# Performance work log

Measured on AMD Instinct MI355X. Metric: run time of the kernel, lower is better.

The kernel has to match this reference:

```python
import jax, jax.numpy as jnp
import numpy as np

D_MODEL = 1024
NUM_HEADS = 16
DEPTH = D_MODEL // NUM_HEADS


def setup_inputs() -> dict:
    key = jax.random.key(0)
    ks = jax.random.split(key, 5)
    s = 1.0 / np.sqrt(D_MODEL)
    return {
        "x": jax.random.normal(ks[0], (4, 2048, D_MODEL), dtype=jnp.float32),
        "wq": jax.random.normal(ks[1], (D_MODEL, D_MODEL), dtype=jnp.float32) * s,
        "bq": jnp.zeros((D_MODEL,), dtype=jnp.float32),
        "wk": jax.random.normal(ks[2], (D_MODEL, D_MODEL), dtype=jnp.float32) * s,
        "bk": jnp.zeros((D_MODEL,), dtype=jnp.float32),
        "wv": jax.random.normal(ks[3], (D_MODEL, D_MODEL), dtype=jnp.float32) * s,
        "bv": jnp.zeros((D_MODEL,), dtype=jnp.float32),
        "wo": jax.random.normal(ks[4], (D_MODEL, D_MODEL), dtype=jnp.float32) * s,
        "bo": jnp.zeros((D_MODEL,), dtype=jnp.float32),
    }


def reference(x, wq, bq, wk, bk, wv, bv, wo, bo):
    B, S, _ = x.shape
    def split_heads(t):  # [B,S,D] -> [B,H,S,depth]
        return t.reshape(B, S, NUM_HEADS, DEPTH).transpose(0, 2, 1, 3)
    q = split_heads(x @ wq + bq)
    k = split_heads(x @ wk + bk)
    v = split_heads(x @ wv + bv)
    scale = 1.0 / jnp.sqrt(jnp.float32(DEPTH))
    logits = jnp.einsum("bhqd,bhkd->bhqk", q, k) * scale
    attn = jax.nn.softmax(logits, axis=-1)  # dropout is identity at inference
    out = jnp.einsum("bhqk,bhkd->bhqd", attn, v)
    out = out.transpose(0, 2, 1, 3).reshape(B, S, D_MODEL)
    return out @ wo + bo
```

## Files before the change

### kernel.cpp

```cpp
#include <hip/hip_runtime.h>
#include <hip/hip_bf16.h>
#include <cstdint>
#include <cstddef>

typedef __attribute__((ext_vector_type(8))) short s8v;
typedef __attribute__((ext_vector_type(4))) float f4v;
typedef __attribute__((ext_vector_type(16))) float f16v;
typedef __attribute__((ext_vector_type(4))) unsigned u4v;

#define MFMA_BF16(a, b, c) __builtin_amdgcn_mfma_f32_16x16x32_bf16((a), (b), (c), 0, 0, 0)
#define MFMA32(a, b, c) __builtin_amdgcn_mfma_f32_32x32x16_bf16((a), (b), (c), 0, 0, 0)

__device__ __forceinline__ short f2bf(float f) {
    unsigned u = __builtin_bit_cast(unsigned, f);
    u += 0x7FFFu + ((u >> 16) & 1u);
    return (short)(u >> 16);
}

__device__ __forceinline__ unsigned cvt_pk_bf16(float a, float b) {
    unsigned r;
    asm("v_cvt_pk_bf16_f32 %0, %1, %2" : "=v"(r) : "v"(a), "v"(b));
    return r;
}

#define GLDS16(gsrc, ldst)                                                                   \
    __builtin_amdgcn_global_load_lds(                                                        \
        (const __attribute__((address_space(1))) unsigned int*)(gsrc),                       \
        (__attribute__((address_space(3))) unsigned int*)(ldst), 16, 0, 0)

__global__ void convert_x(const float4* __restrict__ in, short4* __restrict__ out, int n4) {
    int i = blockIdx.x * blockDim.x + threadIdx.x;
    int stride = gridDim.x * blockDim.x;
    for (; i < n4; i += stride) {
        float4 v = in[i];
        short4 o;
        o.x = f2bf(v.x); o.y = f2bf(v.y); o.z = f2bf(v.z); o.w = f2bf(v.w);
        out[i] = o;
    }
}

__global__ void transpose_w(const float* __restrict__ a0, const float* __restrict__ a1,
                            const float* __restrict__ a2, const float* __restrict__ a3,
                            short* __restrict__ outb) {
    const float* src = (blockIdx.z == 0) ? a0 : (blockIdx.z == 1) ? a1 : (blockIdx.z == 2) ? a2 : a3;
    short* dst = outb + (size_t)blockIdx.z * 1048576;
    __shared__ float t[32][33];
    const int n0 = blockIdx.x * 32, k0 = blockIdx.y * 32;
    const int tid = threadIdx.x;
    const int rr = tid >> 3, c4 = (tid & 7) * 4;
    float4 v = *(const float4*)(src + (size_t)(k0 + rr) * 1024 + n0 + c4);
    t[rr][c4 + 0] = v.x; t[rr][c4 + 1] = v.y; t[rr][c4 + 2] = v.z; t[rr][c4 + 3] = v.w;
    __syncthreads();
    short4 o;
    o.x = f2bf(t[c4 + 0][rr]); o.y = f2bf(t[c4 + 1][rr]);
    o.z = f2bf(t[c4 + 2][rr]); o.w = f2bf(t[c4 + 3][rr]);
    *(short4*)(dst + (size_t)(n0 + rr) * 1024 + k0 + c4) = o;
}

template <typename OUT_T, int MODE>
__global__ __launch_bounds__(256, 2) void gemm_bt(const short* __restrict__ A,
                                                  const short* __restrict__ B,
                                                  const float* __restrict__ bias,
                                                  OUT_T* __restrict__ C,
                                                  int M, int N, int K, float alpha) {
    __shared__ short As[128 * 64];
    __shared__ short Bs[128 * 64];
    const int tid = threadIdx.x;
    const int lane = tid & 63;
    const int w = tid >> 6;
    const int wr = w >> 1, wc = w & 1;
    const int m0 = blockIdx.y * 128, n0 = blockIdx.x * 128;
    const int KB = K * 2;

    f4v acc[4][4] = {};

    for (int kt = 0; kt < K; kt += 64) {
#pragma unroll
        for (int i = 0; i < 4; i++) {
            int o = tid * 16 + i * 4096;
            int r = o >> 7;
            int cs = (o & 127) ^ ((r & 7) << 4);
            GLDS16((const char*)A + (size_t)(m0 + r) * KB + kt * 2 + cs,
                   (char*)As + (w * 1024 + i * 4096));
            GLDS16((const char*)B + (size_t)(n0 + r) * KB + kt * 2 + cs,
                   (char*)Bs + (w * 1024 + i * 4096));
        }
        __syncthreads();
#pragma unroll
        for (int kk = 0; kk < 2; kk++) {
            s8v af[4], bf[4];
#pragma unroll
            for (int mi = 0; mi < 4; mi++) {
                int r = wr * 64 + mi * 16 + (lane & 15);
                int cb = (((lane >> 4) * 16) + kk * 64) ^ ((r & 7) << 4);
                af[mi] = *(const s8v*)((const char*)As + r * 128 + cb);
            }
#pragma unroll
            for (int ni = 0; ni < 4; ni++) {
                int r = wc * 64 + ni * 16 + (lane & 15);
                int cb = (((lane >> 4) * 16) + kk * 64) ^ ((r & 7) << 4);
                bf[ni] = *(const s8v*)((const char*)Bs + r * 128 + cb);
            }
#pragma unroll
            for (int mi = 0; mi < 4; mi++)
#pragma unroll
                for (int ni = 0; ni < 4; ni++)
                    acc[mi][ni] = MFMA_BF16(af[mi], bf[ni], acc[mi][ni]);
        }
        __syncthreads();
    }

#pragma unroll
    for (int mi = 0; mi < 4; mi++) {
#pragma unroll
        for (int ni = 0; ni < 4; ni++) {
            int row = m0 + wr * 64 + mi * 16 + ((lane >> 4) << 2);
            int col = n0 + wc * 64 + ni * 16 + (lane & 15);
#pragma unroll
            for (int j = 0; j < 4; j++) {
                float v = acc[mi][ni][j];
                if constexpr (MODE == 0) {
                    v = (v + bias[col]) * alpha;
                    size_t idx = (size_t)(row + j) * N + col;
                    if constexpr (sizeof(OUT_T) == 2) C[idx] = (OUT_T)f2bf(v);
                    else C[idx] = v;
                } else {
                    v = (v + bias[row + j]) * alpha;
                    size_t idx = (size_t)(col >> 11) * (2048 * 1024) + (size_t)(row + j) * 2048 + (col & 2047);
                    C[idx] = (OUT_T)f2bf(v);
                }
            }
        }
    }
}

__global__ __launch_bounds__(256, 4) void attn_fwd(const short* __restrict__ Qb,
                                                   const short* __restrict__ Kb,
                                                   const short* __restrict__ Vtb,
                                                   short* __restrict__ AOb) {
    __shared__ short Ks[2][64 * 64];
    __shared__ short Vs[2][64 * 64];

    const int tid = threadIdx.x, lane = tid & 63, w = tid >> 6;
    const int l5 = lane & 31, H = lane >> 5;
    const int qt = blockIdx.x;
    const int bh = blockIdx.y;
    const int b = bh >> 4, h = bh & 15;
    const int q0 = qt * 128 + w * 32;

    s8v qf[4];
#pragma unroll
    for (int st = 0; st < 4; st++)
        qf[st] = *(const s8v*)(Qb + (size_t)(b * 2048 + q0 + l5) * 1024 + h * 64 + st * 16 + H * 8);

    f16v oacc[2] = {};
    float l_ = 0.f;

    auto STAGE = [&](int s0, int bi) {
#pragma unroll
        for (int i = 0; i < 2; i++) {
            int o = tid * 16 + i * 4096;
            int r = o >> 7;
            int cs = (o & 127) ^ ((r & 7) << 4);
            GLDS16((const char*)Kb + (size_t)(b * 2048 + s0 + r) * 2048 + h * 128 + cs,
                   (char*)Ks[bi] + w * 1024 + i * 4096);
            GLDS16((const char*)Vtb + (size_t)(b * 1024 + h * 64 + r) * 4096 + (size_t)s0 * 2 + cs,
                   (char*)Vs[bi] + w * 1024 + i * 4096);
        }
    };

    STAGE(0, 0);
    __syncthreads();

    int cur = 0;
    for (int t = 0; t < 32; t++) {
        if (t < 31) STAGE((t + 1) * 64, cur ^ 1);

        f16v sf[2] = {};
        __builtin_amdgcn_s_setprio(1);
#pragma unroll
        for (int kt = 0; kt < 2; kt++) {
            int r = kt * 32 + l5;
            int swz = (r & 7) << 4;
#pragma unroll
            for (int st = 0; st < 4; st++) {
                s8v kf = *(const s8v*)((const char*)Ks[cur] + r * 128 + ((st * 32 + H * 16) ^ swz));
                sf[kt] = MFMA32(kf, qf[st], sf[kt]);
            }
        }
        __builtin_amdgcn_s_setprio(0);

        float rs0 = 0.f, rs1 = 0.f;
#pragma unroll
        for (int kt = 0; kt < 2; kt++)
#pragma unroll
            for (int i = 0; i < 16; i++) {
                float p = __builtin_amdgcn_exp2f(sf[kt][i]);
                sf[kt][i] = p;
                if (i & 1) rs1 += p; else rs0 += p;
            }
        l_ += rs0 + rs1;

#pragma unroll
        for (int s = 0; s < 4; s++) {
            const int kt = s >> 1, base = (s & 1) * 8;
            unsigned dA0 = cvt_pk_bf16(sf[kt][base + 0], sf[kt][base + 1]);
            unsigned dA1 = cvt_pk_bf16(sf[kt][base + 2], sf[kt][base + 3]);
            unsigned dB0 = cvt_pk_bf16(sf[kt][base + 4], sf[kt][base + 5]);
            unsigned dB1 = cvt_pk_bf16(sf[kt][base + 6], sf[kt][base + 7]);
            asm("v_permlane32_swap_b32 %0, %1" : "+v"(dA0), "+v"(dB0));
            asm("v_permlane32_swap_b32 %0, %1" : "+v"(dA1), "+v"(dB1));
            u4v fw = {dA0, dA1, dB0, dB1};
            s8v pfrag = __builtin_bit_cast(s8v, fw);
            __builtin_amdgcn_s_setprio(1);
#pragma unroll
            for (int dt = 0; dt < 2; dt++) {
                int r = dt * 32 + l5;
                s8v vf = *(const s8v*)((const char*)Vs[cur] + r * 128 + ((s * 32 + H * 16) ^ ((r & 7) << 4)));
                oacc[dt] = MFMA32(vf, pfrag, oacc[dt]);
            }
            __builtin_amdgcn_s_setprio(0);
        }
        __syncthreads();
        cur ^= 1;
    }

    float l = l_ + __shfl_xor(l_, 32, 64);
    float rl = 1.0f / l;
    size_t orow = (size_t)(b * 2048 + q0 + l5) * 1024 + h * 64;
#pragma unroll
    for (int dt = 0; dt < 2; dt++)
#pragma unroll
        for (int g = 0; g < 4; g++) {
            short4 o;
            o.x = f2bf(oacc[dt][4 * g + 0] * rl);
            o.y = f2bf(oacc[dt][4 * g + 1] * rl);
            o.z = f2bf(oacc[dt][4 * g + 2] * rl);
            o.w = f2bf(oacc[dt][4 * g + 3] * rl);
            *(short4*)(AOb + orow + dt * 32 + g * 8 + H * 4) = o;
        }
}

extern "C" void kernel_launch(void* const* d_in, const int* in_sizes, int n_in,
                              void* d_out, int out_size, void* d_ws, size_t ws_size,
                              hipStream_t stream) {
    const float* x  = (const float*)d_in[0];
    const float* wq = (const float*)d_in[1];
    const float* bq = (const float*)d_in[2];
    const float* wk = (const float*)d_in[3];
    const float* bk = (const float*)d_in[4];
    const float* wv = (const float*)d_in[5];
    const float* bv = (const float*)d_in[6];
    const float* wo = (const float*)d_in[7];
    const float* bo = (const float*)d_in[8];
    float* out = (float*)d_out;

    char* ws = (char*)d_ws;
    const size_t MB16 = 16777216;
    short* xb  = (short*)(ws);
    short* qb  = (short*)(ws + 1 * MB16);
    short* kb  = (short*)(ws + 2 * MB16);
    short* vtb = (short*)(ws + 3 * MB16);
    short* wT  = (short*)(ws + 4 * MB16);
    short* aob = xb;

    const float qscale = 0.125f * 1.4426950408889634f;

    convert_x<<<dim3(1024), dim3(256), 0, stream>>>((const float4*)x, (short4*)xb, 8388608 / 4);
    transpose_w<<<dim3(32, 32, 4), dim3(256), 0, stream>>>(wq, wk, wv, wo, wT);

    gemm_bt<short, 0><<<dim3(8, 64), dim3(256), 0, stream>>>(xb, wT, bq, qb, 8192, 1024, 1024, qscale);
    gemm_bt<short, 0><<<dim3(8, 64), dim3(256), 0, stream>>>(xb, wT + 1048576, bk, kb, 8192, 1024, 1024, 1.0f);
    gemm_bt<short, 1><<<dim3(64, 8), dim3(256), 0, stream>>>(wT + 2 * 1048576, xb, bv, vtb, 1024, 8192, 1024, 1.0f);

    attn_fwd<<<dim3(16, 64), dim3(256), 0, stream>>>(qb, kb, vtb, aob);

    gemm_bt<float, 0><<<dim3(8, 64), dim3(256), 0, stream>>>(aob, wT + 3 * 1048576, bo, out, 8192, 1024, 1024, 1.0f);
}
```

Before: 199.2 us.

## Fuse QKV projections into one launch and pre-block K for direct register loads

Merges the three Q/K/V projection GEMMs into a single launch that picks its operands and epilogue from blockIdx.x % 3. This removes two launches and lets the three projections share the GPU concurrently. The K projection now writes a blocked layout matching the MFMA fragment order, so the attention kernel loads K fragments straight from global memory into registers. That drops the K shared-memory staging and its LDS traffic, but K reads now go to global/L2 memory on every tile with no double buffering, and the blocked K store scatters 2-byte writes.

```diff
diff --git a/kernel.cpp b/kernel.cpp
--- a/kernel.cpp
+++ b/kernel.cpp
@@ -57,12 +57,102 @@
     *(short4*)(dst + (size_t)(n0 + rr) * 1024 + k0 + c4) = o;
 }
 
-template <typename OUT_T, int MODE>
-__global__ __launch_bounds__(256, 2) void gemm_bt(const short* __restrict__ A,
-                                                  const short* __restrict__ B,
-                                                  const float* __restrict__ bias,
-                                                  OUT_T* __restrict__ C,
-                                                  int M, int N, int K, float alpha) {
+__global__ __launch_bounds__(256, 2) void qkv_gemm(const short* __restrict__ xb,
+                                                   const short* __restrict__ wT,
+                                                   const float* __restrict__ bq,
+                                                   const float* __restrict__ bk,
+                                                   const float* __restrict__ bv,
+                                                   short* __restrict__ qb,
+                                                   short* __restrict__ kblk,
+                                                   short* __restrict__ vtb,
+                                                   float qscale) {
+    __shared__ short As[128 * 64];
+    __shared__ short Bs[128 * 64];
+    const int z = blockIdx.x % 3;
+    const int bxx = blockIdx.x / 3;
+    const int tid = threadIdx.x;
+    const int lane = tid & 63;
+    const int w = tid >> 6;
+    const int wr = w >> 1, wc = w & 1;
+    int m0, n0;
+    const short *A, *B;
+    if (z < 2) { A = xb; B = wT + z * 1048576; m0 = blockIdx.y * 128; n0 = bxx * 128; }
+    else       { A = wT + 2 * 1048576; B = xb; m0 = bxx * 128; n0 = blockIdx.y * 128; }
+
+    f4v acc[4][4] = {};
+
+    for (int kt = 0; kt < 1024; kt += 64) {
+#pragma unroll
+        for (int i = 0; i < 4; i++) {
+            int o = tid * 16 + i * 4096;
+            int r = o >> 7;
+            int cs = (o & 127) ^ ((r & 7) << 4);
+            GLDS16((const char*)A + (size_t)(m0 + r) * 2048 + kt * 2 + cs,
+                   (char*)As + (w * 1024 + i * 4096));
+            GLDS16((const char*)B + (size_t)(n0 + r) * 2048 + kt * 2 + cs,
+                   (char*)Bs + (w * 1024 + i * 4096));
+        }
+        __syncthreads();
+#pragma unroll
+        for (int kk = 0; kk < 2; kk++) {
+            s8v af[4], bf[4];
+#pragma unroll
+            for (int mi = 0; mi < 4; mi++) {
+                int r = wr * 64 + mi * 16 + (lane & 15);
+                int cb = (((lane >> 4) * 16) + kk * 64) ^ ((r & 7) << 4);
+                af[mi] = *(const s8v*)((const char*)As + r * 128 + cb);
+            }
+#pragma unroll
+            for (int ni = 0; ni < 4; ni++) {
+                int r = wc * 64 + ni * 16 + (lane & 15);
+                int cb = (((lane >> 4) * 16) + kk * 64) ^ ((r & 7) << 4);
+                bf[ni] = *(const s8v*)((const char*)Bs + r * 128 + cb);
+            }
+#pragma unroll
+            for (int mi = 0; mi < 4; mi++)
+#pragma unroll
+                for (int ni = 0; ni < 4; ni++)
+                    acc[mi][ni] = MFMA_BF16(af[mi], bf[ni], acc[mi][ni]);
+        }
+        __syncthreads();
+    }
+
+#pragma unroll
+    for (int mi = 0; mi < 4; mi++) {
+#pragma unroll
+        for (int ni = 0; ni < 4; ni++) {
+            int row = m0 + wr * 64 + mi * 16 + ((lane >> 4) << 2);
+            int col = n0 + wc * 64 + ni * 16 + (lane & 15);
+#pragma unroll
+            for (int j = 0; j < 4; j++) {
+                float v = acc[mi][ni][j];
+                if (z == 0) {
+                    v = (v + bq[col]) * qscale;
+                    qb[(size_t)(row + j) * 1024 + col] = f2bf(v);
+                } else if (z == 1) {
+                    v = v + bk[col];
+                    int rs = row + j;
+                    int b = rs >> 11, s_in = rs & 2047;
+                    int t = s_in >> 6, ktb = (s_in >> 5) & 1, l5v = s_in & 31;
+                    int h = col >> 6, dd = col & 63;
+                    int st = dd >> 4, Hh = (dd >> 3) & 1, jj = dd & 7;
+                    size_t kidx = (size_t)(((b * 16 + h) * 32 + t)) * 4096 +
+                                  (ktb * 4 + st) * 512 + (Hh * 32 + l5v) * 8 + jj;
+                    kblk[kidx] = f2bf(v);
+                } else {
+                    v = v + bv[row + j];
+                    size_t idx = (size_t)(col >> 11) * (2048 * 1024) + (size_t)(row + j) * 2048 + (col & 2047);
+                    vtb[idx] = f2bf(v);
+                }
+            }
+        }
+    }
+}
+
+__global__ __launch_bounds__(256, 2) void gemm_o(const short* __restrict__ A,
+                                                 const short* __restrict__ B,
+                                                 const float* __restrict__ bias,
+                                                 float* __restrict__ C) {
     __shared__ short As[128 * 64];
     __shared__ short Bs[128 * 64];
     const int tid = threadIdx.x;
@@ -70,19 +160,18 @@
     const int w = tid >> 6;
     const int wr = w >> 1, wc = w & 1;
     const int m0 = blockIdx.y * 128, n0 = blockIdx.x * 128;
-    const int KB = K * 2;
 
     f4v acc[4][4] = {};
 
-    for (int kt = 0; kt < K; kt += 64) {
+    for (int kt = 0; kt < 1024; kt += 64) {
 #pragma unroll
         for (int i = 0; i < 4; i++) {
             int o = tid * 16 + i * 4096;
             int r = o >> 7;
             int cs = (o & 127) ^ ((r & 7) << 4);
-            GLDS16((const char*)A + (size_t)(m0 + r) * KB + kt * 2 + cs,
+            GLDS16((const char*)A + (size_t)(m0 + r) * 2048 + kt * 2 + cs,
                    (char*)As + (w * 1024 + i * 4096));
-            GLDS16((const char*)B + (size_t)(n0 + r) * KB + kt * 2 + cs,
+            GLDS16((const char*)B + (size_t)(n0 + r) * 2048 + kt * 2 + cs,
                    (char*)Bs + (w * 1024 + i * 4096));
         }
         __syncthreads();
@@ -117,28 +206,16 @@
             int row = m0 + wr * 64 + mi * 16 + ((lane >> 4) << 2);
             int col = n0 + wc * 64 + ni * 16 + (lane & 15);
 #pragma unroll
-            for (int j = 0; j < 4; j++) {
-                float v = acc[mi][ni][j];
-                if constexpr (MODE == 0) {
-                    v = (v + bias[col]) * alpha;
-                    size_t idx = (size_t)(row + j) * N + col;
-                    if constexpr (sizeof(OUT_T) == 2) C[idx] = (OUT_T)f2bf(v);
-                    else C[idx] = v;
-                } else {
-                    v = (v + bias[row + j]) * alpha;
-                    size_t idx = (size_t)(col >> 11) * (2048 * 1024) + (size_t)(row + j) * 2048 + (col & 2047);
-                    C[idx] = (OUT_T)f2bf(v);
-                }
-            }
+            for (int j = 0; j < 4; j++)
+                C[(size_t)(row + j) * 1024 + col] = acc[mi][ni][j] + bias[col];
         }
     }
 }
 
 __global__ __launch_bounds__(256, 4) void attn_fwd(const short* __restrict__ Qb,
-                                                   const short* __restrict__ Kb,
+                                                   const short* __restrict__ Kblk,
                                                    const short* __restrict__ Vtb,
                                                    short* __restrict__ AOb) {
-    __shared__ short Ks[2][64 * 64];
     __shared__ short Vs[2][64 * 64];
 
     const int tid = threadIdx.x, lane = tid & 63, w = tid >> 6;
@@ -153,41 +230,43 @@
     for (int st = 0; st < 4; st++)
         qf[st] = *(const s8v*)(Qb + (size_t)(b * 2048 + q0 + l5) * 1024 + h * 64 + st * 16 + H * 8);
 
+    const short* kbase = Kblk + (size_t)(b * 16 + h) * 131072 + lane * 8;
+
     f16v oacc[2] = {};
     float l_ = 0.f;
 
-    auto STAGE = [&](int s0, int bi) {
+    auto STAGE_V = [&](int s0, int bi) {
 #pragma unroll
         for (int i = 0; i < 2; i++) {
             int o = tid * 16 + i * 4096;
             int r = o >> 7;
             int cs = (o & 127) ^ ((r & 7) << 4);
-            GLDS16((const char*)Kb + (size_t)(b * 2048 + s0 + r) * 2048 + h * 128 + cs,
-                   (char*)Ks[bi] + w * 1024 + i * 4096);
             GLDS16((const char*)Vtb + (size_t)(b * 1024 + h * 64 + r) * 4096 + (size_t)s0 * 2 + cs,
                    (char*)Vs[bi] + w * 1024 + i * 4096);
         }
     };
 
-    STAGE(0, 0);
+    STAGE_V(0, 0);
     __syncthreads();
 
     int cur = 0;
     for (int t = 0; t < 32; t++) {
-        if (t < 31) STAGE((t + 1) * 64, cur ^ 1);
+        if (t < 31) STAGE_V((t + 1) * 64, cur ^ 1);
+
+        s8v kf[2][4];
+#pragma unroll
+        for (int kt = 0; kt < 2; kt++)
+#pragma unroll
+            for (int st = 0; st < 4; st++)
+                kf[kt][st] = *(const s8v*)(kbase + t * 4096 + (kt * 4 + st) * 512);
 
         f16v sf[2] = {};
         __builtin_amdgcn_s_setprio(1);
 #pragma unroll
-        for (int kt = 0; kt < 2; kt++) {
-            int r = kt * 32 + l5;
-            int swz = (r & 7) << 4;
-#pragma unroll
-            for (int st = 0; st < 4; st++) {
-                s8v kf = *(const s8v*)((const char*)Ks[cur] + r * 128 + ((st * 32 + H * 16) ^ swz));
-                sf[kt] = MFMA32(kf, qf[st], sf[kt]);
-            }
-        }
+        for (int kt = 0; kt < 2; kt++)
+#pragma unroll
+            for (int st = 0; st < 4; st++)
+                sf[kt] = MFMA32(kf[kt][st], qf[st], sf[kt]);
         __builtin_amdgcn_s_setprio(0);
 
         float rs0 = 0.f, rs1 = 0.f;
@@ -257,23 +336,21 @@
 
     char* ws = (char*)d_ws;
     const size_t MB16 = 16777216;
-    short* xb  = (short*)(ws);
-    short* qb  = (short*)(ws + 1 * MB16);
-    short* kb  = (short*)(ws + 2 * MB16);
-    short* vtb = (short*)(ws + 3 * MB16);
-    short* wT  = (short*)(ws + 4 * MB16);
-    short* aob = xb;
+    short* xb   = (short*)(ws);
+    short* qb   = (short*)(ws + 1 * MB16);
+    short* kblk = (short*)(ws + 2 * MB16);
+    short* vtb  = (short*)(ws + 3 * MB16);
+    short* wT   = (short*)(ws + 4 * MB16);
+    short* aob  = xb;
 
     const float qscale = 0.125f * 1.4426950408889634f;
 
     convert_x<<<dim3(1024), dim3(256), 0, stream>>>((const float4*)x, (short4*)xb, 8388608 / 4);
     transpose_w<<<dim3(32, 32, 4), dim3(256), 0, stream>>>(wq, wk, wv, wo, wT);
 
-    gemm_bt<short, 0><<<dim3(8, 64), dim3(256), 0, stream>>>(xb, wT, bq, qb, 8192, 1024, 1024, qscale);
-    gemm_bt<short, 0><<<dim3(8, 64), dim3(256), 0, stream>>>(xb, wT + 1048576, bk, kb, 8192, 1024, 1024, 1.0f);
-    gemm_bt<short, 1><<<dim3(64, 8), dim3(256), 0, stream>>>(wT + 2 * 1048576, xb, bv, vtb, 1024, 8192, 1024, 1.0f);
-
-    attn_fwd<<<dim3(16, 64), dim3(256), 0, stream>>>(qb, kb, vtb, aob);
-
-    gemm_bt<float, 0><<<dim3(8, 64), dim3(256), 0, stream>>>(aob, wT + 3 * 1048576, bo, out, 8192, 1024, 1024, 1.0f);
-}
+    qkv_gemm<<<dim3(24, 64), dim3(256), 0, stream>>>(xb, wT, bq, bk, bv, qb, kblk, vtb, qscale);
+
+    attn_fwd<<<dim3(16, 64), dim3(256), 0, stream>>>(qb, kblk, vtb, aob);
+
+    gemm_o<<<dim3(8, 64), dim3(256), 0, stream>>>(aob, wT + 3 * 1048576, bo, out);
+}
```

Measured after the change: 198.0 us. About the same (-0.6%).
